# Performance work log

Measured on AMD Instinct MI355X. Metric: run time of the kernel, lower is better.

## Reference

```python
import jax, jax.numpy as jnp
import numpy as np

E = 64        # first-level branches / experts
N_LEAF = 1024 # leaves per branch (item id = branch*N_LEAF + leaf; zero trajectory = (0,0))
K = 10        # output_list_size


def setup_inputs() -> dict:
    key = jax.random.key(0)
    ks = jax.random.split(key, 8)
    s = 0.05
    B, D, H = 256, 256, 512
    return {
        "state": jax.random.normal(ks[0], (B, D), jnp.float32),
        # root policy (outputs E branch logits)
        "rW1": jax.random.normal(ks[1], (D, H), jnp.float32) * s,
        "rb1": jnp.zeros((H,), jnp.float32),
        "rW2": jax.random.normal(ks[2], (H, H), jnp.float32) * s,
        "rb2": jnp.zeros((H,), jnp.float32),
        "rW3": jax.random.normal(ks[3], (H, E), jnp.float32) * s,
        "rb3": jnp.zeros((E,), jnp.float32),
        # stacked per-branch expert policies (each outputs N_LEAF logits)
        "eW1": jax.random.normal(ks[4], (E, D, H), jnp.float32) * s,
        "eb1": jnp.zeros((E, H), jnp.float32),
        "eW2": jax.random.normal(ks[5], (E, H, H), jnp.float32) * s,
        "eb2": jnp.zeros((E, H), jnp.float32),
        "eW3": jax.random.normal(ks[6], (E, H, N_LEAF), jnp.float32) * s,
        "eb3": jnp.zeros((E, N_LEAF), jnp.float32),
    }


def reference(state, rW1, rb1, rW2, rb2, rW3, rb3, eW1, eb1, eW2, eb2, eW3, eb3):
    # deterministic=True path, mask_items=None
    B = state.shape[0]
    relu = jax.nn.relu
    # root policy: MLP -> branch logits [B, E]
    h = relu(state @ rW1 + rb1)
    h = relu(h @ rW2 + rb2)
    root_logits = h @ rW3 + rb3
    idx = jnp.argmax(root_logits, axis=-1)                       # top-1 branch per sample [B]
    root_lp = jax.nn.log_softmax(root_logits, axis=-1)[jnp.arange(B), idx]  # [B]
    # top-1 routed expert forward: gather per-sample expert weights (MoE dispatch)
    h1 = relu(jnp.einsum('bi,bih->bh', state, eW1[idx]) + eb1[idx])
    h2 = relu(jnp.einsum('bh,bhg->bg', h1, eW2[idx]) + eb2[idx])
    logits = jnp.einsum('bg,bgn->bn', h2, eW3[idx]) + eb3[idx]   # [B, N_LEAF]
    lp = jax.nn.log_softmax(logits, axis=-1)
    # top-(k+1), then drop leaf 0 if this sample routed to branch 0 (the id-0 trajectory)
    _, top_idx = jax.lax.top_k(logits, K + 1)                    # [B, K+1]
    keep = ~((top_idx == 0) & (idx[:, None] == 0))
    order = jnp.argsort(~keep, axis=1, stable=True)              # kept entries first, order preserved
    item_idx = jnp.take_along_axis(top_idx, order[:, :K], axis=1)  # [B, K]
    final_lp = jnp.take_along_axis(lp, item_idx, axis=1) + root_lp[:, None]  # [B, K]
    traj = jnp.stack([jnp.broadcast_to(idx[:, None], (B, K)), item_idx], axis=-1)  # [B, K, 2]
    return traj, final_lp
```

## Files before the change

kernel.cpp:

```cpp
#include <hip/hip_runtime.h>
#include <math.h>

#define Bn 256
#define Dm 256
#define Hm 512
#define Em 64
#define NL 1024
#define TOPK 10
#define GS 8
#define MAXG 88

template<int IN, int OUT, int MT, int CCH, int NW, bool RELU, bool GROUPED>
__global__ __launch_bounds__(NW * 64) void dense_ks(
        const float* __restrict__ X, const int* __restrict__ perm,
        const float* __restrict__ W, const float* __restrict__ Bv,
        const int4* __restrict__ groups, float* __restrict__ Y) {
    constexpr int NT  = NW * 64;
    constexpr int KCH = IN / NW;
    constexpr int NR  = (NW > 4) ? 4 : NW;
    static_assert(CCH == 256 && MT == 8, "");

    int e, p0, cnt;
    if (GROUPED) {
        const int4 g = groups[blockIdx.x];
        if (g.z == 0) return;
        e = g.x; p0 = g.y; cnt = g.z;
    } else {
        e = 0; p0 = blockIdx.x * MT; cnt = MT;
    }

    __shared__ float sxT[IN * MT];
    __shared__ float part[NR * MT * CCH];
    const int tid = threadIdx.x;

    for (int j = tid; j < (IN / 4) * MT; j += NT) {
        const int c  = j & (MT - 1);
        const int i4 = j >> 3;
        float4 x = make_float4(0.f, 0.f, 0.f, 0.f);
        if (c < cnt) {
            int row;
            if (GROUPED) row = perm ? perm[p0 + c] : (p0 + c);
            else         row = p0 + c;
            x = *(const float4*)(X + (size_t)row * IN + i4 * 4);
        }
        sxT[(i4 * 4 + 0) * MT + c] = x.x;
        sxT[(i4 * 4 + 1) * MT + c] = x.y;
        sxT[(i4 * 4 + 2) * MT + c] = x.z;
        sxT[(i4 * 4 + 3) * MT + c] = x.w;
    }
    __syncthreads();

    const int wave = tid >> 6, lane = tid & 63;
    const int colb = blockIdx.y * CCH;
    const int col  = colb + lane * 4;
    const int k0   = wave * KCH;
    const float* We = W + (size_t)e * IN * OUT + (size_t)k0 * OUT + col;

    float acc[MT][4];
    #pragma unroll
    for (int c = 0; c < MT; ++c) { acc[c][0]=0.f; acc[c][1]=0.f; acc[c][2]=0.f; acc[c][3]=0.f; }

    #pragma unroll 4
    for (int i = 0; i < KCH; ++i) {
        const float4 w = *(const float4*)(We + (size_t)i * OUT);
        const float* xr = &sxT[(k0 + i) * MT];
        const float4 xa = *(const float4*)xr;
        const float4 xb = *(const float4*)(xr + 4);
        const float xs[MT] = {xa.x, xa.y, xa.z, xa.w, xb.x, xb.y, xb.z, xb.w};
        #pragma unroll
        for (int c = 0; c < MT; ++c) {
            acc[c][0] = fmaf(xs[c], w.x, acc[c][0]);
            acc[c][1] = fmaf(xs[c], w.y, acc[c][1]);
            acc[c][2] = fmaf(xs[c], w.z, acc[c][2]);
            acc[c][3] = fmaf(xs[c], w.w, acc[c][3]);
        }
    }

    if (wave < NR) {
        #pragma unroll
        for (int c = 0; c < MT; ++c)
            *(float4*)&part[((wave * MT) + c) * CCH + lane * 4] = *(const float4*)acc[c];
    }
    __syncthreads();
    if (NW > NR) {
        if (wave >= NR) {
            #pragma unroll
            for (int c = 0; c < MT; ++c) {
                float4* p = (float4*)&part[(((wave - NR) * MT) + c) * CCH + lane * 4];
                float4 v = *p;
                v.x += acc[c][0]; v.y += acc[c][1]; v.z += acc[c][2]; v.w += acc[c][3];
                *p = v;
            }
        }
        __syncthreads();
    }

    for (int j = tid; j < MT * (CCH / 4); j += NT) {
        const int c = j / (CCH / 4);
        const int q = j % (CCH / 4);
        float4 s = *(const float4*)&part[c * CCH + q * 4];
        #pragma unroll
        for (int w = 1; w < NR; ++w) {
            const float4 p = *(const float4*)&part[((w * MT) + c) * CCH + q * 4];
            s.x += p.x; s.y += p.y; s.z += p.z; s.w += p.w;
        }
        if (c < cnt) {
            const float4 b = *(const float4*)(Bv + (size_t)e * OUT + colb + q * 4);
            s.x += b.x; s.y += b.y; s.z += b.z; s.w += b.w;
            if (RELU) {
                s.x = fmaxf(s.x, 0.f); s.y = fmaxf(s.y, 0.f);
                s.z = fmaxf(s.z, 0.f); s.w = fmaxf(s.w, 0.f);
            }
            *(float4*)(Y + (size_t)(p0 + c) * OUT + colb + q * 4) = s;
        }
    }
}

__global__ __launch_bounds__(512) void root3_ks(
        const float* __restrict__ H2, const float* __restrict__ W,
        const float* __restrict__ bias, int* __restrict__ idx_out,
        float* __restrict__ rlp_out) {
    __shared__ float sxT[Hm * 8];
    __shared__ float part[8 * 8 * Em];
    __shared__ float fin[8][Em];
    const int tid = threadIdx.x;
    const int b0 = blockIdx.x * 8;

    for (int j = tid; j < (Hm / 4) * 8; j += 512) {
        const int c = j & 7, i4 = j >> 3;
        const float4 x = *(const float4*)(H2 + (size_t)(b0 + c) * Hm + i4 * 4);
        sxT[(i4 * 4 + 0) * 8 + c] = x.x;
        sxT[(i4 * 4 + 1) * 8 + c] = x.y;
        sxT[(i4 * 4 + 2) * 8 + c] = x.z;
        sxT[(i4 * 4 + 3) * 8 + c] = x.w;
    }
    __syncthreads();

    const int wave = tid >> 6, lane = tid & 63;
    const int k0 = wave * 64;
    float acc[8] = {0.f,0.f,0.f,0.f,0.f,0.f,0.f,0.f};
    #pragma unroll 4
    for (int i = 0; i < 64; ++i) {
        const float w = W[(size_t)(k0 + i) * Em + lane];
        const float* xr = &sxT[(k0 + i) * 8];
        const float4 xa = *(const float4*)xr;
        const float4 xb = *(const float4*)(xr + 4);
        acc[0] = fmaf(xa.x, w, acc[0]); acc[1] = fmaf(xa.y, w, acc[1]);
        acc[2] = fmaf(xa.z, w, acc[2]); acc[3] = fmaf(xa.w, w, acc[3]);
        acc[4] = fmaf(xb.x, w, acc[4]); acc[5] = fmaf(xb.y, w, acc[5]);
        acc[6] = fmaf(xb.z, w, acc[6]); acc[7] = fmaf(xb.w, w, acc[7]);
    }
    #pragma unroll
    for (int c = 0; c < 8; ++c) part[(wave * 8 + c) * Em + lane] = acc[c];
    __syncthreads();

    {
        const int c = wave, colj = lane;
        float s = bias[colj];
        #pragma unroll
        for (int w = 0; w < 8; ++w) s += part[(w * 8 + c) * Em + colj];
        fin[c][colj] = s;
    }
    __syncthreads();

    {
        const int c = wave;
        const float a0 = fin[c][lane];
        float v = a0; int bi = lane;
        #pragma unroll
        for (int off = 32; off; off >>= 1) {
            const float ov = __shfl_xor(v, off);
            const int   oi = __shfl_xor(bi, off);
            if (ov > v || (ov == v && oi < bi)) { v = ov; bi = oi; }
        }
        float ssum = expf(a0 - v);
        #pragma unroll
        for (int off = 32; off; off >>= 1) ssum += __shfl_xor(ssum, off);
        if (lane == 0) { idx_out[b0 + c] = bi; rlp_out[b0 + c] = -logf(ssum); }
    }
}

__global__ void routing_kernel(const int* __restrict__ idx, int* __restrict__ perm,
                               int4* __restrict__ groups) {
    __shared__ int cnt[Em];
    __shared__ int offs[Em];
    const int tid = threadIdx.x;
    if (tid < Em) cnt[tid] = 0;
    __syncthreads();
    const int e = idx[tid];
    const int r = atomicAdd(&cnt[e], 1);
    __syncthreads();
    if (tid == 0) {
        int run = 0, g = 0;
        for (int ee = 0; ee < Em; ++ee) {
            offs[ee] = run;
            const int n = cnt[ee];
            for (int k = 0; k < n; k += GS)
                groups[g++] = make_int4(ee, run + k, min(GS, n - k), 0);
            run += n;
        }
        for (; g < MAXG; ++g) groups[g] = make_int4(0, 0, 0, 0);
    }
    __syncthreads();
    perm[offs[e] + r] = tid;
}

__global__ __launch_bounds__(256) void topk_kernel(
        const float* __restrict__ logits, const int* __restrict__ perm,
        const int* __restrict__ idx, const float* __restrict__ rlp,
        float* __restrict__ out) {
    __shared__ float sl[NL];
    __shared__ float redA[4];
    __shared__ float redB[4];
    __shared__ float bcast[2];
    const int p = blockIdx.x;
    const int tid = threadIdx.x;
    const int b = perm[p];
    const int e = idx[b];
    const float* row = logits + (size_t)p * NL;

    const float4 v4 = *(const float4*)(row + tid * 4);
    *(float4*)&sl[tid * 4] = v4;

    float m = fmaxf(fmaxf(v4.x, v4.y), fmaxf(v4.z, v4.w));
    #pragma unroll
    for (int off = 32; off; off >>= 1) m = fmaxf(m, __shfl_xor(m, off));
    const int wid = tid >> 6;
    if ((tid & 63) == 0) redA[wid] = m;
    __syncthreads();
    if (tid == 0) {
        float mm = redA[0];
        #pragma unroll
        for (int w = 1; w < 4; ++w) mm = fmaxf(mm, redA[w]);
        bcast[0] = mm;
    }
    __syncthreads();
    m = bcast[0];

    float s = expf(v4.x - m) + expf(v4.y - m) + expf(v4.z - m) + expf(v4.w - m);
    #pragma unroll
    for (int off = 32; off; off >>= 1) s += __shfl_xor(s, off);
    if ((tid & 63) == 0) redB[wid] = s;
    __syncthreads();
    if (tid == 0) {
        float ss = 0.f;
        #pragma unroll
        for (int w = 0; w < 4; ++w) ss += redB[w];
        bcast[1] = m + logf(ss);
    }
    __syncthreads();
    const float logZ = bcast[1];

    if (tid < 64) {
        float vals[16];
        #pragma unroll
        for (int q = 0; q < 16; ++q) vals[q] = sl[tid * 16 + q];
        float selv[11];
        int   seli[11];
        for (int t = 0; t < 11; ++t) {
            float v = -INFINITY; int bq = 0;
            #pragma unroll
            for (int q = 0; q < 16; ++q) {
                if (vals[q] > v) { v = vals[q]; bq = q; }
            }
            int gi = tid * 16 + bq;
            #pragma unroll
            for (int off = 32; off; off >>= 1) {
                const float ov = __shfl_xor(v, off);
                const int   oi = __shfl_xor(gi, off);
                if (ov > v || (ov == v && oi < gi)) { v = ov; gi = oi; }
            }
            selv[t] = v;
            seli[t] = gi;
            if ((gi >> 4) == tid) vals[gi & 15] = -INFINITY;
        }
        if (tid == 0) {
            const float rl = rlp[b];
            int cnt = 0;
            for (int t = 0; t < 11 && cnt < TOPK; ++t) {
                if (seli[t] == 0 && e == 0) continue;
                out[(b * TOPK + cnt) * 2 + 0] = (float)e;
                out[(b * TOPK + cnt) * 2 + 1] = (float)seli[t];
                out[Bn * TOPK * 2 + b * TOPK + cnt] = selv[t] - logZ + rl;
                ++cnt;
            }
        }
    }
}

extern "C" void kernel_launch(void* const* d_in, const int* in_sizes, int n_in,
                              void* d_out, int out_size, void* d_ws, size_t ws_size,
                              hipStream_t stream) {
    const float* state = (const float*)d_in[0];
    const float* rW1   = (const float*)d_in[1];
    const float* rb1   = (const float*)d_in[2];
    const float* rW2   = (const float*)d_in[3];
    const float* rb2   = (const float*)d_in[4];
    const float* rW3   = (const float*)d_in[5];
    const float* rb3   = (const float*)d_in[6];
    const float* eW1   = (const float*)d_in[7];
    const float* eb1   = (const float*)d_in[8];
    const float* eW2   = (const float*)d_in[9];
    const float* eb2   = (const float*)d_in[10];
    const float* eW3   = (const float*)d_in[11];
    const float* eb3   = (const float*)d_in[12];
    float* out = (float*)d_out;

    float* eh1    = (float*)d_ws;
    float* eh2    = eh1 + Bn * Hm;
    float* logits = eh2 + Bn * Hm;
    float* rlp    = logits + Bn * NL;
    int*   idxp   = (int*)(rlp + Bn);
    int*   perm   = idxp + Bn;
    int4*  groups = (int4*)(perm + Bn);
    float* rh1 = eh1;
    float* rh2 = logits;

    dense_ks<Dm, Hm, 8, 256, 4, true, false><<<dim3(Bn / 8, Hm / 256), 256, 0, stream>>>(
        state, nullptr, rW1, rb1, nullptr, rh1);
    dense_ks<Hm, Hm, 8, 256, 8, true, false><<<dim3(Bn / 8, Hm / 256), 512, 0, stream>>>(
        rh1, nullptr, rW2, rb2, nullptr, rh2);
    root3_ks<<<Bn / 8, 512, 0, stream>>>(rh2, rW3, rb3, idxp, rlp);
    routing_kernel<<<1, 256, 0, stream>>>(idxp, perm, groups);
    dense_ks<Dm, Hm, 8, 256, 4, true, true><<<dim3(MAXG, Hm / 256), 256, 0, stream>>>(
        state, perm, eW1, eb1, groups, eh1);
    dense_ks<Hm, Hm, 8, 256, 8, true, true><<<dim3(MAXG, Hm / 256), 512, 0, stream>>>(
        eh1, nullptr, eW2, eb2, groups, eh2);
    dense_ks<Hm, NL, 8, 256, 8, false, true><<<dim3(MAXG, NL / 256), 512, 0, stream>>>(
        eh2, nullptr, eW3, eb3, groups, logits);
    topk_kernel<<<Bn, 256, 0, stream>>>(logits, perm, idxp, rlp, out);
}
```

Measured before the change: 97.24 us.

## Fuse all stages into one cooperative persistent kernel with grid syncs

```diff
diff --git a/kernel.cpp b/kernel.cpp
--- a/kernel.cpp
+++ b/kernel.cpp
@@ -1,5 +1,8 @@
 #include <hip/hip_runtime.h>
+#include <hip/hip_cooperative_groups.h>
 #include <math.h>
+
+namespace cg = cooperative_groups;
 
 #define Bn 256
 #define Dm 256
@@ -9,38 +12,35 @@
 #define TOPK 10
 #define GS 8
 #define MAXG 88
-
-template<int IN, int OUT, int MT, int CCH, int NW, bool RELU, bool GROUPED>
-__global__ __launch_bounds__(NW * 64) void dense_ks(
+#define NBLK 256
+#define NTHR 512
+
+struct Params {
+    const float* state;
+    const float* rW1; const float* rb1;
+    const float* rW2; const float* rb2;
+    const float* rW3; const float* rb3;
+    const float* eW1; const float* eb1;
+    const float* eW2; const float* eb2;
+    const float* eW3; const float* eb3;
+    float* out;
+    float* h1; float* h2; float* logits;
+    float* rlp; int* idxp; int* perm; int4* groups;
+};
+
+template<int IN, int OUT, int MT>
+__device__ __forceinline__ void dense_unit(
         const float* __restrict__ X, const int* __restrict__ perm,
         const float* __restrict__ W, const float* __restrict__ Bv,
-        const int4* __restrict__ groups, float* __restrict__ Y) {
-    constexpr int NT  = NW * 64;
-    constexpr int KCH = IN / NW;
-    constexpr int NR  = (NW > 4) ? 4 : NW;
-    static_assert(CCH == 256 && MT == 8, "");
-
-    int e, p0, cnt;
-    if (GROUPED) {
-        const int4 g = groups[blockIdx.x];
-        if (g.z == 0) return;
-        e = g.x; p0 = g.y; cnt = g.z;
-    } else {
-        e = 0; p0 = blockIdx.x * MT; cnt = MT;
-    }
-
-    __shared__ float sxT[IN * MT];
-    __shared__ float part[NR * MT * CCH];
-    const int tid = threadIdx.x;
-
-    for (int j = tid; j < (IN / 4) * MT; j += NT) {
+        int e, int p0, int cnt, int colb, bool relu,
+        float* sxT, float* part, int tid, float* __restrict__ Y) {
+    constexpr int NW = 8, KCH = IN / NW, CCH = 256, NR = 4;
+    for (int j = tid; j < (IN / 4) * MT; j += NTHR) {
         const int c  = j & (MT - 1);
-        const int i4 = j >> 3;
+        const int i4 = j / MT;
         float4 x = make_float4(0.f, 0.f, 0.f, 0.f);
         if (c < cnt) {
-            int row;
-            if (GROUPED) row = perm ? perm[p0 + c] : (p0 + c);
-            else         row = p0 + c;
+            const int row = perm ? perm[p0 + c] : (p0 + c);
             x = *(const float4*)(X + (size_t)row * IN + i4 * 4);
         }
         sxT[(i4 * 4 + 0) * MT + c] = x.x;
@@ -51,9 +51,8 @@
     __syncthreads();
 
     const int wave = tid >> 6, lane = tid & 63;
-    const int colb = blockIdx.y * CCH;
-    const int col  = colb + lane * 4;
-    const int k0   = wave * KCH;
+    const int col = colb + lane * 4;
+    const int k0 = wave * KCH;
     const float* We = W + (size_t)e * IN * OUT + (size_t)k0 * OUT + col;
 
     float acc[MT][4];
@@ -64,15 +63,27 @@
     for (int i = 0; i < KCH; ++i) {
         const float4 w = *(const float4*)(We + (size_t)i * OUT);
         const float* xr = &sxT[(k0 + i) * MT];
-        const float4 xa = *(const float4*)xr;
-        const float4 xb = *(const float4*)(xr + 4);
-        const float xs[MT] = {xa.x, xa.y, xa.z, xa.w, xb.x, xb.y, xb.z, xb.w};
-        #pragma unroll
-        for (int c = 0; c < MT; ++c) {
-            acc[c][0] = fmaf(xs[c], w.x, acc[c][0]);
-            acc[c][1] = fmaf(xs[c], w.y, acc[c][1]);
-            acc[c][2] = fmaf(xs[c], w.z, acc[c][2]);
-            acc[c][3] = fmaf(xs[c], w.w, acc[c][3]);
+        if constexpr (MT == 8) {
+            const float4 xa = *(const float4*)xr;
+            const float4 xb = *(const float4*)(xr + 4);
+            const float xs[8] = {xa.x, xa.y, xa.z, xa.w, xb.x, xb.y, xb.z, xb.w};
+            #pragma unroll
+            for (int c = 0; c < 8; ++c) {
+                acc[c][0] = fmaf(xs[c], w.x, acc[c][0]);
+                acc[c][1] = fmaf(xs[c], w.y, acc[c][1]);
+                acc[c][2] = fmaf(xs[c], w.z, acc[c][2]);
+                acc[c][3] = fmaf(xs[c], w.w, acc[c][3]);
+            }
+        } else {
+            const float4 xa = *(const float4*)xr;
+            const float xs[4] = {xa.x, xa.y, xa.z, xa.w};
+            #pragma unroll
+            for (int c = 0; c < 4; ++c) {
+                acc[c][0] = fmaf(xs[c], w.x, acc[c][0]);
+                acc[c][1] = fmaf(xs[c], w.y, acc[c][1]);
+                acc[c][2] = fmaf(xs[c], w.z, acc[c][2]);
+                acc[c][3] = fmaf(xs[c], w.w, acc[c][3]);
+            }
         }
     }
 
@@ -82,32 +93,30 @@
             *(float4*)&part[((wave * MT) + c) * CCH + lane * 4] = *(const float4*)acc[c];
     }
     __syncthreads();
-    if (NW > NR) {
-        if (wave >= NR) {
-            #pragma unroll
-            for (int c = 0; c < MT; ++c) {
-                float4* p = (float4*)&part[(((wave - NR) * MT) + c) * CCH + lane * 4];
-                float4 v = *p;
-                v.x += acc[c][0]; v.y += acc[c][1]; v.z += acc[c][2]; v.w += acc[c][3];
-                *p = v;
-            }
-        }
-        __syncthreads();
-    }
-
-    for (int j = tid; j < MT * (CCH / 4); j += NT) {
+    if (wave >= NR) {
+        #pragma unroll
+        for (int c = 0; c < MT; ++c) {
+            float4* pp = (float4*)&part[(((wave - NR) * MT) + c) * CCH + lane * 4];
+            float4 v = *pp;
+            v.x += acc[c][0]; v.y += acc[c][1]; v.z += acc[c][2]; v.w += acc[c][3];
+            *pp = v;
+        }
+    }
+    __syncthreads();
+
+    for (int j = tid; j < MT * (CCH / 4); j += NTHR) {
         const int c = j / (CCH / 4);
         const int q = j % (CCH / 4);
         float4 s = *(const float4*)&part[c * CCH + q * 4];
         #pragma unroll
         for (int w = 1; w < NR; ++w) {
-            const float4 p = *(const float4*)&part[((w * MT) + c) * CCH + q * 4];
-            s.x += p.x; s.y += p.y; s.z += p.z; s.w += p.w;
+            const float4 p2 = *(const float4*)&part[((w * MT) + c) * CCH + q * 4];
+            s.x += p2.x; s.y += p2.y; s.z += p2.z; s.w += p2.w;
         }
         if (c < cnt) {
             const float4 b = *(const float4*)(Bv + (size_t)e * OUT + colb + q * 4);
             s.x += b.x; s.y += b.y; s.z += b.z; s.w += b.w;
-            if (RELU) {
+            if (relu) {
                 s.x = fmaxf(s.x, 0.f); s.y = fmaxf(s.y, 0.f);
                 s.z = fmaxf(s.z, 0.f); s.w = fmaxf(s.w, 0.f);
             }
@@ -116,17 +125,15 @@
     }
 }
 
-__global__ __launch_bounds__(512) void root3_ks(
-        const float* __restrict__ H2, const float* __restrict__ W,
-        const float* __restrict__ bias, int* __restrict__ idx_out,
+__device__ __forceinline__ void root3_unit(const float* __restrict__ H2,
+        const float* __restrict__ W, const float* __restrict__ bias,
+        int tile, int tid, float* smem, int* __restrict__ idx_out,
         float* __restrict__ rlp_out) {
-    __shared__ float sxT[Hm * 8];
-    __shared__ float part[8 * 8 * Em];
-    __shared__ float fin[8][Em];
-    const int tid = threadIdx.x;
-    const int b0 = blockIdx.x * 8;
-
-    for (int j = tid; j < (Hm / 4) * 8; j += 512) {
+    float* sxT  = smem;
+    float* part = smem + 4096;
+    float* fin  = smem + 8192;
+    const int b0 = tile * 8;
+    for (int j = tid; j < (Hm / 4) * 8; j += NTHR) {
         const int c = j & 7, i4 = j >> 3;
         const float4 x = *(const float4*)(H2 + (size_t)(b0 + c) * Hm + i4 * 4);
         sxT[(i4 * 4 + 0) * 8 + c] = x.x;
@@ -135,7 +142,6 @@
         sxT[(i4 * 4 + 3) * 8 + c] = x.w;
     }
     __syncthreads();
-
     const int wave = tid >> 6, lane = tid & 63;
     const int k0 = wave * 64;
     float acc[8] = {0.f,0.f,0.f,0.f,0.f,0.f,0.f,0.f};
@@ -153,19 +159,17 @@
     #pragma unroll
     for (int c = 0; c < 8; ++c) part[(wave * 8 + c) * Em + lane] = acc[c];
     __syncthreads();
-
     {
         const int c = wave, colj = lane;
         float s = bias[colj];
         #pragma unroll
         for (int w = 0; w < 8; ++w) s += part[(w * 8 + c) * Em + colj];
-        fin[c][colj] = s;
-    }
-    __syncthreads();
-
+        fin[c * Em + colj] = s;
+    }
+    __syncthreads();
     {
         const int c = wave;
-        const float a0 = fin[c][lane];
+        const float a0 = fin[c * Em + lane];
         float v = a0; int bi = lane;
         #pragma unroll
         for (int off = 32; off; off >>= 1) {
@@ -180,15 +184,14 @@
     }
 }
 
-__global__ void routing_kernel(const int* __restrict__ idx, int* __restrict__ perm,
-                               int4* __restrict__ groups) {
-    __shared__ int cnt[Em];
-    __shared__ int offs[Em];
-    const int tid = threadIdx.x;
+__device__ __forceinline__ void routing_unit(const int* __restrict__ idx,
+        int* __restrict__ perm, int4* __restrict__ groups, int tid, float* smem) {
+    int* cnt  = (int*)smem;
+    int* offs = (int*)smem + 64;
     if (tid < Em) cnt[tid] = 0;
     __syncthreads();
-    const int e = idx[tid];
-    const int r = atomicAdd(&cnt[e], 1);
+    int e = -1, r = -1;
+    if (tid < Bn) { e = idx[tid]; r = atomicAdd(&cnt[e], 1); }
     __syncthreads();
     if (tid == 0) {
         int run = 0, g = 0;
@@ -202,50 +205,47 @@
         for (; g < MAXG; ++g) groups[g] = make_int4(0, 0, 0, 0);
     }
     __syncthreads();
-    perm[offs[e] + r] = tid;
-}
-
-__global__ __launch_bounds__(256) void topk_kernel(
-        const float* __restrict__ logits, const int* __restrict__ perm,
-        const int* __restrict__ idx, const float* __restrict__ rlp,
+    if (tid < Bn) perm[offs[e] + r] = tid;
+}
+
+__device__ __forceinline__ void topk_unit(const float* __restrict__ logits,
+        const int* __restrict__ perm, const int* __restrict__ idx,
+        const float* __restrict__ rlp, int p, int tid, float* smem,
         float* __restrict__ out) {
-    __shared__ float sl[NL];
-    __shared__ float redA[4];
-    __shared__ float redB[4];
-    __shared__ float bcast[2];
-    const int p = blockIdx.x;
-    const int tid = threadIdx.x;
+    float* sl    = smem;
+    float* redA  = smem + 1024;
+    float* redB  = smem + 1032;
+    float* bcast = smem + 1040;
     const int b = perm[p];
     const int e = idx[b];
     const float* row = logits + (size_t)p * NL;
-
-    const float4 v4 = *(const float4*)(row + tid * 4);
-    *(float4*)&sl[tid * 4] = v4;
-
-    float m = fmaxf(fmaxf(v4.x, v4.y), fmaxf(v4.z, v4.w));
+    const float2 v2 = *(const float2*)(row + tid * 2);
+    sl[tid * 2] = v2.x; sl[tid * 2 + 1] = v2.y;
+
+    float m = fmaxf(v2.x, v2.y);
     #pragma unroll
     for (int off = 32; off; off >>= 1) m = fmaxf(m, __shfl_xor(m, off));
-    const int wid = tid >> 6;
-    if ((tid & 63) == 0) redA[wid] = m;
+    const int wave = tid >> 6;
+    if ((tid & 63) == 0) redA[wave] = m;
     __syncthreads();
     if (tid == 0) {
         float mm = redA[0];
         #pragma unroll
-        for (int w = 1; w < 4; ++w) mm = fmaxf(mm, redA[w]);
+        for (int w = 1; w < 8; ++w) mm = fmaxf(mm, redA[w]);
         bcast[0] = mm;
     }
     __syncthreads();
     m = bcast[0];
 
-    float s = expf(v4.x - m) + expf(v4.y - m) + expf(v4.z - m) + expf(v4.w - m);
+    float s = expf(v2.x - m) + expf(v2.y - m);
     #pragma unroll
     for (int off = 32; off; off >>= 1) s += __shfl_xor(s, off);
-    if ((tid & 63) == 0) redB[wid] = s;
+    if ((tid & 63) == 0) redB[wave] = s;
     __syncthreads();
     if (tid == 0) {
         float ss = 0.f;
         #pragma unroll
-        for (int w = 0; w < 4; ++w) ss += redB[w];
+        for (int w = 0; w < 8; ++w) ss += redB[w];
         bcast[1] = m + logf(ss);
     }
     __syncthreads();
@@ -276,57 +276,90 @@
         }
         if (tid == 0) {
             const float rl = rlp[b];
-            int cnt = 0;
-            for (int t = 0; t < 11 && cnt < TOPK; ++t) {
+            int c2 = 0;
+            for (int t = 0; t < 11 && c2 < TOPK; ++t) {
                 if (seli[t] == 0 && e == 0) continue;
-                out[(b * TOPK + cnt) * 2 + 0] = (float)e;
-                out[(b * TOPK + cnt) * 2 + 1] = (float)seli[t];
-                out[Bn * TOPK * 2 + b * TOPK + cnt] = selv[t] - logZ + rl;
-                ++cnt;
-            }
-        }
-    }
+                out[(b * TOPK + c2) * 2 + 0] = (float)e;
+                out[(b * TOPK + c2) * 2 + 1] = (float)seli[t];
+                out[Bn * TOPK * 2 + b * TOPK + c2] = selv[t] - logZ + rl;
+                ++c2;
+            }
+        }
+    }
+}
+
+__global__ __launch_bounds__(NTHR) void mega_kernel(Params P) {
+    cg::grid_group grid = cg::this_grid();
+    __shared__ float smem[12288];
+    float* sxT  = smem;
+    float* part = smem + 4096;
+    const int tid = threadIdx.x;
+    const int bid = blockIdx.x;
+
+    if (bid < 128) {
+        const int tile = bid & 63, cgp = bid >> 6;
+        dense_unit<Dm, Hm, 4>(P.state, nullptr, P.rW1, P.rb1, 0, tile * 4, 4,
+                              cgp * 256, true, sxT, part, tid, P.h1);
+    }
+    grid.sync();
+    if (bid < 128) {
+        const int tile = bid & 63, cgp = bid >> 6;
+        dense_unit<Hm, Hm, 4>(P.h1, nullptr, P.rW2, P.rb2, 0, tile * 4, 4,
+                              cgp * 256, true, sxT, part, tid, P.h2);
+    }
+    grid.sync();
+    if (bid < 32) root3_unit(P.h2, P.rW3, P.rb3, bid, tid, smem, P.idxp, P.rlp);
+    grid.sync();
+    if (bid == 0) routing_unit(P.idxp, P.perm, P.groups, tid, smem);
+    grid.sync();
+    if (bid < 176) {
+        const int grp = bid >> 1, cgp = bid & 1;
+        const int4 gr = P.groups[grp];
+        if (gr.z) dense_unit<Dm, Hm, 8>(P.state, P.perm, P.eW1, P.eb1, gr.x, gr.y, gr.z,
+                                        cgp * 256, true, sxT, part, tid, P.h1);
+    }
+    grid.sync();
+    if (bid < 176) {
+        const int grp = bid >> 1, cgp = bid & 1;
+        const int4 gr = P.groups[grp];
+        if (gr.z) dense_unit<Hm, Hm, 8>(P.h1, nullptr, P.eW2, P.eb2, gr.x, gr.y, gr.z,
+                                        cgp * 256, true, sxT, part, tid, P.h2);
+    }
+    grid.sync();
+    for (int u = bid; u < MAXG * 4; u += NBLK) {
+        const int grp = u >> 2, cgp = u & 3;
+        const int4 gr = P.groups[grp];
+        if (gr.z) dense_unit<Hm, NL, 8>(P.h2, nullptr, P.eW3, P.eb3, gr.x, gr.y, gr.z,
+                                        cgp * 256, false, sxT, part, tid, P.logits);
+    }
+    grid.sync();
+    topk_unit(P.logits, P.perm, P.idxp, P.rlp, bid, tid, smem, P.out);
 }
 
 extern "C" void kernel_launch(void* const* d_in, const int* in_sizes, int n_in,
                               void* d_out, int out_size, void* d_ws, size_t ws_size,
                               hipStream_t stream) {
-    const float* state = (const float*)d_in[0];
-    const float* rW1   = (const float*)d_in[1];
-    const float* rb1   = (const float*)d_in[2];
-    const float* rW2   = (const float*)d_in[3];
-    const float* rb2   = (const float*)d_in[4];
-    const float* rW3   = (const float*)d_in[5];
-    const float* rb3   = (const float*)d_in[6];
-    const float* eW1   = (const float*)d_in[7];
-    const float* eb1   = (const float*)d_in[8];
-    const float* eW2   = (const float*)d_in[9];
-    const float* eb2   = (const float*)d_in[10];
-    const float* eW3   = (const float*)d_in[11];
-    const float* eb3   = (const float*)d_in[12];
-    float* out = (float*)d_out;
-
-    float* eh1    = (float*)d_ws;
-    float* eh2    = eh1 + Bn * Hm;
-    float* logits = eh2 + Bn * Hm;
+    Params P;
+    P.state = (const float*)d_in[0];
+    P.rW1 = (const float*)d_in[1];  P.rb1 = (const float*)d_in[2];
+    P.rW2 = (const float*)d_in[3];  P.rb2 = (const float*)d_in[4];
+    P.rW3 = (const float*)d_in[5];  P.rb3 = (const float*)d_in[6];
+    P.eW1 = (const float*)d_in[7];  P.eb1 = (const float*)d_in[8];
+    P.eW2 = (const float*)d_in[9];  P.eb2 = (const float*)d_in[10];
+    P.eW3 = (const float*)d_in[11]; P.eb3 = (const float*)d_in[12];
+    P.out = (float*)d_out;
+
+    float* h1     = (float*)d_ws;
+    float* h2     = h1 + Bn * Hm;
+    float* logits = h2 + Bn * Hm;
     float* rlp    = logits + Bn * NL;
     int*   idxp   = (int*)(rlp + Bn);
     int*   perm   = idxp + Bn;
     int4*  groups = (int4*)(perm + Bn);
-    float* rh1 = eh1;
-    float* rh2 = logits;
-
-    dense_ks<Dm, Hm, 8, 256, 4, true, false><<<dim3(Bn / 8, Hm / 256), 256, 0, stream>>>(
-        state, nullptr, rW1, rb1, nullptr, rh1);
-    dense_ks<Hm, Hm, 8, 256, 8, true, false><<<dim3(Bn / 8, Hm / 256), 512, 0, stream>>>(
-        rh1, nullptr, rW2, rb2, nullptr, rh2);
-    root3_ks<<<Bn / 8, 512, 0, stream>>>(rh2, rW3, rb3, idxp, rlp);
-    routing_kernel<<<1, 256, 0, stream>>>(idxp, perm, groups);
-    dense_ks<Dm, Hm, 8, 256, 4, true, true><<<dim3(MAXG, Hm / 256), 256, 0, stream>>>(
-        state, perm, eW1, eb1, groups, eh1);
-    dense_ks<Hm, Hm, 8, 256, 8, true, true><<<dim3(MAXG, Hm / 256), 512, 0, stream>>>(
-        eh1, nullptr, eW2, eb2, groups, eh2);
-    dense_ks<Hm, NL, 8, 256, 8, false, true><<<dim3(MAXG, NL / 256), 512, 0, stream>>>(
-        eh2, nullptr, eW3, eb3, groups, logits);
-    topk_kernel<<<Bn, 256, 0, stream>>>(logits, perm, idxp, rlp, out);
-}
+    P.h1 = h1; P.h2 = h2; P.logits = logits;
+    P.rlp = rlp; P.idxp = idxp; P.perm = perm; P.groups = groups;
+
+    void* args[] = { &P };
+    hipLaunchCooperativeKernel((const void*)mega_kernel, dim3(NBLK), dim3(NTHR),
+                               args, 0, stream);
+}
```

New measurement: 262.0 us. 2.69x slower.

## Split-K dense layers with atomic accumulation and defer bias/ReLU to consumers

Applied to the files above, without the earlier changes.

```diff
diff --git a/kernel.cpp b/kernel.cpp
--- a/kernel.cpp
+++ b/kernel.cpp
@@ -10,15 +10,18 @@
 #define GS 8
 #define MAXG 88
 
-template<int IN, int OUT, int MT, int CCH, int NW, bool RELU, bool GROUPED>
-__global__ __launch_bounds__(NW * 64) void dense_ks(
+__global__ __launch_bounds__(256) void zero_kernel(float* __restrict__ p, int n4) {
+    const int i = blockIdx.x * 256 + threadIdx.x;
+    if (i < n4) ((float4*)p)[i] = make_float4(0.f, 0.f, 0.f, 0.f);
+}
+
+template<int IN, int OUT, int MT, bool GROUPED>
+__global__ __launch_bounds__(512) void dense_ks2(
         const float* __restrict__ X, const int* __restrict__ perm,
-        const float* __restrict__ W, const float* __restrict__ Bv,
-        const int4* __restrict__ groups, float* __restrict__ Y) {
-    constexpr int NT  = NW * 64;
-    constexpr int KCH = IN / NW;
-    constexpr int NR  = (NW > 4) ? 4 : NW;
-    static_assert(CCH == 256 && MT == 8, "");
+        const float* __restrict__ Bin, size_t bin_estride,
+        const float* __restrict__ W, const int4* __restrict__ groups,
+        float* __restrict__ Y) {
+    constexpr int NW = 8, KHALF = IN / 2, KCH = KHALF / NW, CCH = 256, NR = 4;
 
     int e, p0, cnt;
     if (GROUPED) {
@@ -28,20 +31,25 @@
     } else {
         e = 0; p0 = blockIdx.x * MT; cnt = MT;
     }
-
-    __shared__ float sxT[IN * MT];
+    const int kh = blockIdx.z;
+    const int kbase = kh * KHALF;
+
+    __shared__ float sxT[KHALF * MT];
     __shared__ float part[NR * MT * CCH];
     const int tid = threadIdx.x;
 
-    for (int j = tid; j < (IN / 4) * MT; j += NT) {
+    for (int j = tid; j < (KHALF / 4) * MT; j += 512) {
         const int c  = j & (MT - 1);
-        const int i4 = j >> 3;
+        const int i4 = j / MT;
         float4 x = make_float4(0.f, 0.f, 0.f, 0.f);
         if (c < cnt) {
-            int row;
-            if (GROUPED) row = perm ? perm[p0 + c] : (p0 + c);
-            else         row = p0 + c;
-            x = *(const float4*)(X + (size_t)row * IN + i4 * 4);
+            const int row = (GROUPED && perm) ? perm[p0 + c] : (p0 + c);
+            x = *(const float4*)(X + (size_t)row * IN + kbase + i4 * 4);
+            if (Bin) {
+                const float4 b = *(const float4*)(Bin + (size_t)e * bin_estride + kbase + i4 * 4);
+                x.x = fmaxf(x.x + b.x, 0.f); x.y = fmaxf(x.y + b.y, 0.f);
+                x.z = fmaxf(x.z + b.z, 0.f); x.w = fmaxf(x.w + b.w, 0.f);
+            }
         }
         sxT[(i4 * 4 + 0) * MT + c] = x.x;
         sxT[(i4 * 4 + 1) * MT + c] = x.y;
@@ -54,7 +62,7 @@
     const int colb = blockIdx.y * CCH;
     const int col  = colb + lane * 4;
     const int k0   = wave * KCH;
-    const float* We = W + (size_t)e * IN * OUT + (size_t)k0 * OUT + col;
+    const float* We = W + (size_t)e * IN * OUT + (size_t)(kbase + k0) * OUT + col;
 
     float acc[MT][4];
     #pragma unroll
@@ -64,15 +72,27 @@
     for (int i = 0; i < KCH; ++i) {
         const float4 w = *(const float4*)(We + (size_t)i * OUT);
         const float* xr = &sxT[(k0 + i) * MT];
-        const float4 xa = *(const float4*)xr;
-        const float4 xb = *(const float4*)(xr + 4);
-        const float xs[MT] = {xa.x, xa.y, xa.z, xa.w, xb.x, xb.y, xb.z, xb.w};
-        #pragma unroll
-        for (int c = 0; c < MT; ++c) {
-            acc[c][0] = fmaf(xs[c], w.x, acc[c][0]);
-            acc[c][1] = fmaf(xs[c], w.y, acc[c][1]);
-            acc[c][2] = fmaf(xs[c], w.z, acc[c][2]);
-            acc[c][3] = fmaf(xs[c], w.w, acc[c][3]);
+        if constexpr (MT == 8) {
+            const float4 xa = *(const float4*)xr;
+            const float4 xb = *(const float4*)(xr + 4);
+            const float xs[8] = {xa.x, xa.y, xa.z, xa.w, xb.x, xb.y, xb.z, xb.w};
+            #pragma unroll
+            for (int c = 0; c < 8; ++c) {
+                acc[c][0] = fmaf(xs[c], w.x, acc[c][0]);
+                acc[c][1] = fmaf(xs[c], w.y, acc[c][1]);
+                acc[c][2] = fmaf(xs[c], w.z, acc[c][2]);
+                acc[c][3] = fmaf(xs[c], w.w, acc[c][3]);
+            }
+        } else {
+            const float4 xa = *(const float4*)xr;
+            const float xs[4] = {xa.x, xa.y, xa.z, xa.w};
+            #pragma unroll
+            for (int c = 0; c < 4; ++c) {
+                acc[c][0] = fmaf(xs[c], w.x, acc[c][0]);
+                acc[c][1] = fmaf(xs[c], w.y, acc[c][1]);
+                acc[c][2] = fmaf(xs[c], w.z, acc[c][2]);
+                acc[c][3] = fmaf(xs[c], w.w, acc[c][3]);
+            }
         }
     }
 
@@ -82,44 +102,40 @@
             *(float4*)&part[((wave * MT) + c) * CCH + lane * 4] = *(const float4*)acc[c];
     }
     __syncthreads();
-    if (NW > NR) {
-        if (wave >= NR) {
-            #pragma unroll
-            for (int c = 0; c < MT; ++c) {
-                float4* p = (float4*)&part[(((wave - NR) * MT) + c) * CCH + lane * 4];
-                float4 v = *p;
-                v.x += acc[c][0]; v.y += acc[c][1]; v.z += acc[c][2]; v.w += acc[c][3];
-                *p = v;
-            }
-        }
-        __syncthreads();
-    }
-
-    for (int j = tid; j < MT * (CCH / 4); j += NT) {
+    if (wave >= NR) {
+        #pragma unroll
+        for (int c = 0; c < MT; ++c) {
+            float4* pp = (float4*)&part[(((wave - NR) * MT) + c) * CCH + lane * 4];
+            float4 v = *pp;
+            v.x += acc[c][0]; v.y += acc[c][1]; v.z += acc[c][2]; v.w += acc[c][3];
+            *pp = v;
+        }
+    }
+    __syncthreads();
+
+    for (int j = tid; j < MT * (CCH / 4); j += 512) {
         const int c = j / (CCH / 4);
         const int q = j % (CCH / 4);
         float4 s = *(const float4*)&part[c * CCH + q * 4];
         #pragma unroll
         for (int w = 1; w < NR; ++w) {
-            const float4 p = *(const float4*)&part[((w * MT) + c) * CCH + q * 4];
-            s.x += p.x; s.y += p.y; s.z += p.z; s.w += p.w;
+            const float4 p2 = *(const float4*)&part[((w * MT) + c) * CCH + q * 4];
+            s.x += p2.x; s.y += p2.y; s.z += p2.z; s.w += p2.w;
         }
         if (c < cnt) {
-            const float4 b = *(const float4*)(Bv + (size_t)e * OUT + colb + q * 4);
-            s.x += b.x; s.y += b.y; s.z += b.z; s.w += b.w;
-            if (RELU) {
-                s.x = fmaxf(s.x, 0.f); s.y = fmaxf(s.y, 0.f);
-                s.z = fmaxf(s.z, 0.f); s.w = fmaxf(s.w, 0.f);
-            }
-            *(float4*)(Y + (size_t)(p0 + c) * OUT + colb + q * 4) = s;
+            float* yp = Y + (size_t)(p0 + c) * OUT + colb + q * 4;
+            atomicAdd(yp + 0, s.x);
+            atomicAdd(yp + 1, s.y);
+            atomicAdd(yp + 2, s.z);
+            atomicAdd(yp + 3, s.w);
         }
     }
 }
 
 __global__ __launch_bounds__(512) void root3_ks(
-        const float* __restrict__ H2, const float* __restrict__ W,
-        const float* __restrict__ bias, int* __restrict__ idx_out,
-        float* __restrict__ rlp_out) {
+        const float* __restrict__ H2, const float* __restrict__ Bin,
+        const float* __restrict__ W, const float* __restrict__ bias,
+        int* __restrict__ idx_out, float* __restrict__ rlp_out) {
     __shared__ float sxT[Hm * 8];
     __shared__ float part[8 * 8 * Em];
     __shared__ float fin[8][Em];
@@ -128,7 +144,10 @@
 
     for (int j = tid; j < (Hm / 4) * 8; j += 512) {
         const int c = j & 7, i4 = j >> 3;
-        const float4 x = *(const float4*)(H2 + (size_t)(b0 + c) * Hm + i4 * 4);
+        float4 x = *(const float4*)(H2 + (size_t)(b0 + c) * Hm + i4 * 4);
+        const float4 b = *(const float4*)(Bin + i4 * 4);
+        x.x = fmaxf(x.x + b.x, 0.f); x.y = fmaxf(x.y + b.y, 0.f);
+        x.z = fmaxf(x.z + b.z, 0.f); x.w = fmaxf(x.w + b.w, 0.f);
         sxT[(i4 * 4 + 0) * 8 + c] = x.x;
         sxT[(i4 * 4 + 1) * 8 + c] = x.y;
         sxT[(i4 * 4 + 2) * 8 + c] = x.z;
@@ -153,7 +172,6 @@
     #pragma unroll
     for (int c = 0; c < 8; ++c) part[(wave * 8 + c) * Em + lane] = acc[c];
     __syncthreads();
-
     {
         const int c = wave, colj = lane;
         float s = bias[colj];
@@ -162,7 +180,6 @@
         fin[c][colj] = s;
     }
     __syncthreads();
-
     {
         const int c = wave;
         const float a0 = fin[c][lane];
@@ -205,13 +222,13 @@
     perm[offs[e] + r] = tid;
 }
 
-__global__ __launch_bounds__(256) void topk_kernel(
-        const float* __restrict__ logits, const int* __restrict__ perm,
-        const int* __restrict__ idx, const float* __restrict__ rlp,
-        float* __restrict__ out) {
+__global__ __launch_bounds__(512) void topk_kernel(
+        const float* __restrict__ logits, const float* __restrict__ eb3,
+        const int* __restrict__ perm, const int* __restrict__ idx,
+        const float* __restrict__ rlp, float* __restrict__ out) {
     __shared__ float sl[NL];
-    __shared__ float redA[4];
-    __shared__ float redB[4];
+    __shared__ float redA[8];
+    __shared__ float redB[8];
     __shared__ float bcast[2];
     const int p = blockIdx.x;
     const int tid = threadIdx.x;
@@ -219,33 +236,35 @@
     const int e = idx[b];
     const float* row = logits + (size_t)p * NL;
 
-    const float4 v4 = *(const float4*)(row + tid * 4);
-    *(float4*)&sl[tid * 4] = v4;
-
-    float m = fmaxf(fmaxf(v4.x, v4.y), fmaxf(v4.z, v4.w));
+    float2 v2 = *(const float2*)(row + tid * 2);
+    const float2 b2 = *(const float2*)(eb3 + (size_t)e * NL + tid * 2);
+    v2.x += b2.x; v2.y += b2.y;
+    sl[tid * 2] = v2.x; sl[tid * 2 + 1] = v2.y;
+
+    float m = fmaxf(v2.x, v2.y);
     #pragma unroll
     for (int off = 32; off; off >>= 1) m = fmaxf(m, __shfl_xor(m, off));
-    const int wid = tid >> 6;
-    if ((tid & 63) == 0) redA[wid] = m;
+    const int wave = tid >> 6;
+    if ((tid & 63) == 0) redA[wave] = m;
     __syncthreads();
     if (tid == 0) {
         float mm = redA[0];
         #pragma unroll
-        for (int w = 1; w < 4; ++w) mm = fmaxf(mm, redA[w]);
+        for (int w = 1; w < 8; ++w) mm = fmaxf(mm, redA[w]);
         bcast[0] = mm;
     }
     __syncthreads();
     m = bcast[0];
 
-    float s = expf(v4.x - m) + expf(v4.y - m) + expf(v4.z - m) + expf(v4.w - m);
+    float s = expf(v2.x - m) + expf(v2.y - m);
     #pragma unroll
     for (int off = 32; off; off >>= 1) s += __shfl_xor(s, off);
-    if ((tid & 63) == 0) redB[wid] = s;
+    if ((tid & 63) == 0) redB[wave] = s;
     __syncthreads();
     if (tid == 0) {
         float ss = 0.f;
         #pragma unroll
-        for (int w = 0; w < 4; ++w) ss += redB[w];
+        for (int w = 0; w < 8; ++w) ss += redB[w];
         bcast[1] = m + logf(ss);
     }
     __syncthreads();
@@ -276,13 +295,13 @@
         }
         if (tid == 0) {
             const float rl = rlp[b];
-            int cnt = 0;
-            for (int t = 0; t < 11 && cnt < TOPK; ++t) {
+            int c2 = 0;
+            for (int t = 0; t < 11 && c2 < TOPK; ++t) {
                 if (seli[t] == 0 && e == 0) continue;
-                out[(b * TOPK + cnt) * 2 + 0] = (float)e;
-                out[(b * TOPK + cnt) * 2 + 1] = (float)seli[t];
-                out[Bn * TOPK * 2 + b * TOPK + cnt] = selv[t] - logZ + rl;
-                ++cnt;
+                out[(b * TOPK + c2) * 2 + 0] = (float)e;
+                out[(b * TOPK + c2) * 2 + 1] = (float)seli[t];
+                out[Bn * TOPK * 2 + b * TOPK + c2] = selv[t] - logZ + rl;
+                ++c2;
             }
         }
     }
@@ -306,27 +325,30 @@
     const float* eb3   = (const float*)d_in[12];
     float* out = (float*)d_out;
 
-    float* eh1    = (float*)d_ws;
+    float* h1r    = (float*)d_ws;
+    float* h2r    = h1r + Bn * Hm;
+    float* eh1    = h2r + Bn * Hm;
     float* eh2    = eh1 + Bn * Hm;
     float* logits = eh2 + Bn * Hm;
     float* rlp    = logits + Bn * NL;
     int*   idxp   = (int*)(rlp + Bn);
     int*   perm   = idxp + Bn;
     int4*  groups = (int4*)(perm + Bn);
-    float* rh1 = eh1;
-    float* rh2 = logits;
-
-    dense_ks<Dm, Hm, 8, 256, 4, true, false><<<dim3(Bn / 8, Hm / 256), 256, 0, stream>>>(
-        state, nullptr, rW1, rb1, nullptr, rh1);
-    dense_ks<Hm, Hm, 8, 256, 8, true, false><<<dim3(Bn / 8, Hm / 256), 512, 0, stream>>>(
-        rh1, nullptr, rW2, rb2, nullptr, rh2);
-    root3_ks<<<Bn / 8, 512, 0, stream>>>(rh2, rW3, rb3, idxp, rlp);
+
+    const int zero_f = Bn * Hm * 4 + Bn * NL;
+    zero_kernel<<<zero_f / 4 / 256, 256, 0, stream>>>(h1r, zero_f / 4);
+
+    dense_ks2<Dm, Hm, 8, false><<<dim3(Bn / 8, Hm / 256, 2), 512, 0, stream>>>(
+        state, nullptr, nullptr, 0, rW1, nullptr, h1r);
+    dense_ks2<Hm, Hm, 8, false><<<dim3(Bn / 8, Hm / 256, 2), 512, 0, stream>>>(
+        h1r, nullptr, rb1, 0, rW2, nullptr, h2r);
+    root3_ks<<<Bn / 8, 512, 0, stream>>>(h2r, rb2, rW3, rb3, idxp, rlp);
     routing_kernel<<<1, 256, 0, stream>>>(idxp, perm, groups);
-    dense_ks<Dm, Hm, 8, 256, 4, true, true><<<dim3(MAXG, Hm / 256), 256, 0, stream>>>(
-        state, perm, eW1, eb1, groups, eh1);
-    dense_ks<Hm, Hm, 8, 256, 8, true, true><<<dim3(MAXG, Hm / 256), 512, 0, stream>>>(
-        eh1, nullptr, eW2, eb2, groups, eh2);
-    dense_ks<Hm, NL, 8, 256, 8, false, true><<<dim3(MAXG, NL / 256), 512, 0, stream>>>(
-        eh2, nullptr, eW3, eb3, groups, logits);
-    topk_kernel<<<Bn, 256, 0, stream>>>(logits, perm, idxp, rlp, out);
-}
+    dense_ks2<Dm, Hm, 8, true><<<dim3(MAXG, Hm / 256, 2), 512, 0, stream>>>(
+        state, perm, nullptr, 0, eW1, groups, eh1);
+    dense_ks2<Hm, Hm, 8, true><<<dim3(MAXG, Hm / 256, 2), 512, 0, stream>>>(
+        eh1, nullptr, eb1, Hm, eW2, groups, eh2);
+    dense_ks2<Hm, NL, 8, true><<<dim3(MAXG, NL / 256, 2), 512, 0, stream>>>(
+        eh2, nullptr, eb2, Hm, eW3, groups, logits);
+    topk_kernel<<<Bn, 512, 0, stream>>>(logits, eb3, perm, idxp, rlp, out);
+}
```

Measured after the change: 105.5 us. 1.09x slower.
